# Optimization experiments

Measured on AMD Instinct MI355X. Metric: run time of the kernel, lower is better.

The kernel has to match this reference:

```python
import jax, jax.numpy as jnp
from jax import lax
import numpy as np

ALPHA = 1.0
GAMMA = 1e-6
KBLK = 64  # codebook block size for the L1 NN search scan


def setup_inputs() -> dict:
    key = jax.random.key(0)
    ks = jax.random.split(key, 6)
    B, T, C, F, D, K = 8, 1024, 32, 256, 128, 512
    return {
        "X": jax.random.normal(ks[0], (B, T, C), jnp.float32),
        "H": jax.random.normal(ks[1], (B, D, T), jnp.float32),
        "M": jax.random.normal(ks[2], (D, K), jnp.float32),
        "Hdec": jax.random.normal(ks[3], (B, T, F), jnp.float32),
        "W": jax.random.normal(ks[4], (C, F), jnp.float32) * 0.05,
        "w_d": jax.random.normal(ks[5], (C,), jnp.float32) * 0.05,
    }


def _memory_loss(H, M):
    # H: [B, D, T], M: [D, K]
    Ht = jnp.transpose(H, (0, 2, 1))            # [B, T, D]
    MT = M.T                                     # [K, D] codewords
    K, D = MT.shape
    nblk = K // KBLK
    blocks = MT.reshape(nblk, KBLK, D)
    bases = jnp.arange(nblk, dtype=jnp.int32) * KBLK

    def step(carry, blk_base):
        best_d, best_i = carry
        blk, base = blk_base
        # L1 distance to this block of codewords: [B, T, KBLK]
        d = jnp.sum(jnp.abs(Ht[:, :, None, :] - blk[None, None, :, :]), axis=-1)
        bd = jnp.min(d, axis=-1)
        bi = jnp.argmin(d, axis=-1).astype(jnp.int32) + base
        upd = bd < best_d  # strict < keeps the first (lowest-index) argmin, as torch does
        return (jnp.where(upd, bd, best_d), jnp.where(upd, bi, best_i)), None

    init = (jnp.full(Ht.shape[:2], jnp.inf, Ht.dtype),
            jnp.zeros(Ht.shape[:2], jnp.int32))
    (_, best_i), _ = lax.scan(step, init, (blocks, bases))

    Zt = MT[best_i]  # [B, T, D] gathered nearest codewords
    sg = lax.stop_gradient
    # sum of per-(b,d) squared L2 norms over T == total squared sum
    diffs = jnp.sum((sg(Ht) - Zt) ** 2) + jnp.sum((Ht - sg(Zt)) ** 2)
    return diffs / float(np.prod(H.shape))


def reference(X, H, M, Hdec, W, w_d):
    # decoder last layer + discriminator head (needed for adaptive weight grads)
    def rec_loss(w):
        Xhat = jnp.einsum('btf,cf->btc', Hdec, w)
        return jnp.mean((Xhat - X) ** 2)

    def d_loss(w):
        Xhat = jnp.einsum('btf,cf->btc', Hdec, w)
        return -jnp.mean(Xhat @ w_d)

    loss_rec = rec_loss(W)
    loss_d = d_loss(W)
    loss_m = _memory_loss(H, M)

    g_rec = jax.grad(rec_loss)(W)
    g_d = jax.grad(d_loss)(W)
    lmbda = lax.stop_gradient(
        jnp.linalg.norm(g_rec) / (jnp.linalg.norm(g_d) + GAMMA))

    return loss_rec + ALPHA * loss_m + lmbda * loss_d
```

## Files before the change

kernel.cpp:

```cpp
#include <hip/hip_runtime.h>
#include <hip/hip_bf16.h>
#include <math.h>

#define N_POS 8192
#define D_DIM 128
#define K_DIM 512
#define C_DIM 32
#define F_DIM 256
#define NKT   4
#define GREC_COLS 8448
#define L2_BLOCKS 388
#define XG_BLOCKS 256

__device__ __forceinline__ float block_reduce_256(float v) {
    __shared__ float sbuf[4];
    __syncthreads();
#pragma unroll
    for (int off = 32; off > 0; off >>= 1) v += __shfl_down(v, off);
    const int lane = threadIdx.x & 63;
    const int w    = threadIdx.x >> 6;
    if (lane == 0) sbuf[w] = v;
    __syncthreads();
    return (threadIdx.x == 0) ? (sbuf[0] + sbuf[1] + sbuf[2] + sbuf[3]) : 0.f;
}

__global__ __launch_bounds__(256, 4)
void fused_l1(const float* __restrict__ H, const float* __restrict__ M,
              const float* __restrict__ Hdec, const float* __restrict__ W,
              const float* __restrict__ X, const float* __restrict__ w_d,
              float* __restrict__ MT, float* __restrict__ pd,
              int* __restrict__ pi, float* __restrict__ pp,
              float* __restrict__ accum) {
    __shared__ __align__(16) char smem_raw[38912];
    const int tid = threadIdx.x;

    if (blockIdx.x >= XG_BLOCKS) {
        float* hT = (float*)smem_raw;
        float* mT = hT + 2048;
        float* rd = hT;
        int*   ri = (int*)(hT + 1024);

        const int nb    = blockIdx.x - XG_BLOCKS;
        const int ptile = nb >> 2;
        const int ktile = nb & 3;
        const int pos0  = ptile << 6;
        const int b     = pos0 >> 10;
        const int t0    = pos0 & 1023;
        const int k0    = ktile << 7;
        const float* Hb = H + (b << 17) + t0;

        const int hq = (tid & 15) << 2;
        const int hr = tid >> 4;
        const int mq = (tid & 31) << 2;
        const int mr = tid >> 5;
        const int p4 = (tid & 15) << 2;
        const int q4 = (tid >> 4) << 2;

        float acc[4][8];
#pragma unroll
        for (int i = 0; i < 4; ++i)
#pragma unroll
            for (int j = 0; j < 8; ++j) acc[i][j] = 0.f;

        auto absacc32 = [&](const float4& A,
                            const float4& Ma, const float4& Mc) {
            const float hh[4] = {A.x,  A.y,  A.z,  A.w};
            const float mm[8] = {Ma.x, Ma.y, Ma.z, Ma.w, Mc.x, Mc.y, Mc.z, Mc.w};
#pragma unroll
            for (int i = 0; i < 4; ++i)
#pragma unroll
                for (int j = 0; j < 8; ++j) {
                    const float dv = hh[i] - mm[j];
                    asm("v_add_f32 %0, %0, abs(%1)"
                        : "+v"(acc[i][j]) : "v"(dv));
                }
        };

        const float* hrow = hT + p4;
        const float* mrow = mT + q4;

        for (int ch = 0; ch < 4; ++ch) {
            const int d0 = ch << 5;
            __syncthreads();
#pragma unroll
            for (int p = 0; p < 2; ++p) {
                const int d = (p << 4) + hr;
                *(float4*)(hT + (d << 6) + hq) =
                    *(const float4*)(Hb + ((size_t)(d0 + d) << 10) + hq);
            }
#pragma unroll
            for (int p = 0; p < 4; ++p) {
                const int d = (p << 3) + mr;
                *(float4*)(mT + (d << 7) + mq) =
                    *(const float4*)(M + (size_t)(d0 + d) * K_DIM + k0 + mq);
            }
            __syncthreads();

            float4 ha = *(const float4*)(hrow);
            float4 ma = *(const float4*)(mrow);
            float4 mc = *(const float4*)(mrow + 64);
#pragma unroll 2
            for (int d = 0; d < 31; ++d) {
                const float4 nha = *(const float4*)(hrow + ((d + 1) << 6));
                const float4 nma = *(const float4*)(mrow + ((d + 1) << 7));
                const float4 nmc = *(const float4*)(mrow + ((d + 1) << 7) + 64);
                absacc32(ha, ma, mc);
                ha = nha; ma = nma; mc = nmc;
            }
            absacc32(ha, ma, mc);
        }

        __syncthreads();

#pragma unroll
        for (int i = 0; i < 4; ++i) {
            const int pl = p4 + i;
            float bd = acc[i][0];
            int   bj = 0;
#pragma unroll
            for (int j = 1; j < 8; ++j)
                if (acc[i][j] < bd) { bd = acc[i][j]; bj = j; }
            const int bk = k0 + ((bj < 4) ? (q4 + bj) : (64 + q4 + bj - 4));
            rd[(tid >> 4) * 64 + pl] = bd;
            ri[(tid >> 4) * 64 + pl] = bk;
        }
        __syncthreads();

        if (tid < 64) {
            float bd = rd[tid];
            int   bi = ri[tid];
#pragma unroll
            for (int q = 1; q < 16; ++q) {
                const float d = rd[q * 64 + tid];
                const int   k = ri[q * 64 + tid];
                if (d < bd || (d == bd && k < bi)) { bd = d; bi = k; }
            }
            pd[ktile * N_POS + pos0 + tid] = bd;
            pi[ktile * N_POS + pos0 + tid] = bi;
        }
    } else {
        float* Wl = (float*)smem_raw;
        float* El = Wl + C_DIM * 260;
        const int xb  = blockIdx.x;
        const int bt0 = xb << 5;

        if (xb < 64) {
            const int d0 = xb << 1;
            const int d  = d0 + (tid >> 7);
            const int k  = (tid & 127) << 2;
#pragma unroll
            for (int j = 0; j < 4; ++j)
                MT[(size_t)(k + j) * D_DIM + d] = M[(size_t)d * K_DIM + k + j];
        }

#pragma unroll
        for (int it = 0; it < 8; ++it) {
            const int i = it * 1024 + tid * 4;
            const float4 v = *(const float4*)(W + i);
            *(float4*)(Wl + (i >> 8) * 260 + (i & 255)) = v;
        }
        __syncthreads();

        const int c  = tid & 31;
        const int rg = tid >> 5;
        const int r0 = bt0 + rg, r1 = r0 + 8, r2 = r0 + 16, r3 = r0 + 24;

        float a0 = 0.f, a1 = 0.f, a2 = 0.f, a3 = 0.f;
#pragma unroll 4
        for (int f0 = 0; f0 < F_DIM; f0 += 4) {
            const float4 w4 = *(const float4*)(Wl + c * 260 + f0);
            const float4 h0 = *(const float4*)(Hdec + (size_t)r0 * F_DIM + f0);
            const float4 h1 = *(const float4*)(Hdec + (size_t)r1 * F_DIM + f0);
            const float4 h2 = *(const float4*)(Hdec + (size_t)r2 * F_DIM + f0);
            const float4 h3 = *(const float4*)(Hdec + (size_t)r3 * F_DIM + f0);
            a0 += h0.x * w4.x + h0.y * w4.y + h0.z * w4.z + h0.w * w4.w;
            a1 += h1.x * w4.x + h1.y * w4.y + h1.z * w4.z + h1.w * w4.w;
            a2 += h2.x * w4.x + h2.y * w4.y + h2.z * w4.z + h2.w * w4.w;
            a3 += h3.x * w4.x + h3.y * w4.y + h3.z * w4.z + h3.w * w4.w;
        }

        const float wd = w_d[c];
        const float e0 = a0 - X[(size_t)r0 * C_DIM + c];
        const float e1 = a1 - X[(size_t)r1 * C_DIM + c];
        const float e2 = a2 - X[(size_t)r2 * C_DIM + c];
        const float e3 = a3 - X[(size_t)r3 * C_DIM + c];
        El[(rg)      * 32 + c] = e0;
        El[(rg + 8)  * 32 + c] = e1;
        El[(rg + 16) * 32 + c] = e2;
        El[(rg + 24) * 32 + c] = e3;
        const float sse = e0 * e0 + e1 * e1 + e2 * e2 + e3 * e3;
        const float dp  = (a0 + a1 + a2 + a3) * wd;
        const float rA = block_reduce_256(sse);
        if (tid == 0) atomicAdd(accum + 0, rA);
        const float rB = block_reduce_256(dp);
        if (tid == 0) atomicAdd(accum + 1, rB);
        __syncthreads();

        const int f = tid;
        const float* hp = Hdec + (size_t)bt0 * F_DIM + f;
        float gacc[C_DIM];
#pragma unroll
        for (int cc = 0; cc < C_DIM; ++cc) gacc[cc] = 0.f;
        float sf = 0.f;
        float hd0 = hp[0];
        float hd1 = hp[F_DIM];
#pragma unroll 1
        for (int i = 0; i < 30; ++i) {
            const float hdn = hp[(size_t)(i + 2) * F_DIM];
            sf += hd0;
#pragma unroll
            for (int c4 = 0; c4 < 8; ++c4) {
                const float4 e4 = *(const float4*)(El + i * 32 + c4 * 4);
                gacc[c4 * 4 + 0] += e4.x * hd0;
                gacc[c4 * 4 + 1] += e4.y * hd0;
                gacc[c4 * 4 + 2] += e4.z * hd0;
                gacc[c4 * 4 + 3] += e4.w * hd0;
            }
            hd0 = hd1; hd1 = hdn;
        }
#pragma unroll
        for (int i = 30; i < 32; ++i) {
            sf += hd0;
#pragma unroll
            for (int c4 = 0; c4 < 8; ++c4) {
                const float4 e4 = *(const float4*)(El + i * 32 + c4 * 4);
                gacc[c4 * 4 + 0] += e4.x * hd0;
                gacc[c4 * 4 + 1] += e4.y * hd0;
                gacc[c4 * 4 + 2] += e4.z * hd0;
                gacc[c4 * 4 + 3] += e4.w * hd0;
            }
            hd0 = hd1;
        }
        float* o = pp + (size_t)xb * GREC_COLS;
#pragma unroll
        for (int cc = 0; cc < C_DIM; ++cc) o[cc * F_DIM + f] = gacc[cc];
        o[8192 + f] = sf;
    }
}

__global__ __launch_bounds__(256)
void fused_l2(const float* __restrict__ H, const float* __restrict__ MT,
              const float* __restrict__ pd, const int* __restrict__ pi,
              const float* __restrict__ pp, const float* __restrict__ w_d,
              float* __restrict__ accum, float* __restrict__ out) {
    const int tid = threadIdx.x;
    if (blockIdx.x < 256) {
        const int bx = blockIdx.x & 31;
        const int by = blockIdx.x >> 5;
        const int pos = bx * 256 + tid;
        const int b = pos >> 10;
        const int t = pos & 1023;

        const int d0 = by * 16;
        const float* Hb = H + (b << 17) + t + (d0 << 10);
        float hv[16];
#pragma unroll
        for (int j = 0; j < 16; ++j) hv[j] = Hb[j << 10];

        float bd = INFINITY;
        int   bi = 0x7fffffff;
#pragma unroll
        for (int p = 0; p < NKT; ++p) {
            const float d = pd[p * N_POS + pos];
            const int   k = pi[p * N_POS + pos];
            if (d < bd || (d == bd && k < bi)) { bd = d; bi = k; }
        }

        const float* z  = MT + (size_t)bi * D_DIM + d0;
        const float4 z0 = *(const float4*)(z);
        const float4 z1 = *(const float4*)(z + 4);
        const float4 z2 = *(const float4*)(z + 8);
        const float4 z3 = *(const float4*)(z + 12);
        float s0 = 0.f, s1 = 0.f, s2 = 0.f, s3 = 0.f;
        float e;
        e = hv[0]  - z0.x; s0 += e * e;
        e = hv[1]  - z0.y; s1 += e * e;
        e = hv[2]  - z0.z; s2 += e * e;
        e = hv[3]  - z0.w; s3 += e * e;
        e = hv[4]  - z1.x; s0 += e * e;
        e = hv[5]  - z1.y; s1 += e * e;
        e = hv[6]  - z1.z; s2 += e * e;
        e = hv[7]  - z1.w; s3 += e * e;
        e = hv[8]  - z2.x; s0 += e * e;
        e = hv[9]  - z2.y; s1 += e * e;
        e = hv[10] - z2.z; s2 += e * e;
        e = hv[11] - z2.w; s3 += e * e;
        e = hv[12] - z3.x; s0 += e * e;
        e = hv[13] - z3.y; s1 += e * e;
        e = hv[14] - z3.z; s2 += e * e;
        e = hv[15] - z3.w; s3 += e * e;
        const float r = block_reduce_256((s0 + s1) + (s2 + s3));
        if (tid == 0) atomicAdd(accum + 2, r);
    } else {
        const int g = blockIdx.x - 256;
        const int col = (g < 128) ? (g * 64 + (tid & 63))
                                  : (8192 + (g - 128) * 64 + (tid & 63));
        const int pc  = tid >> 6;
        const float* base = pp + (size_t)(pc * 64) * GREC_COLS + col;
        float s = 0.f;
#pragma unroll 8
        for (int p = 0; p < 64; ++p) s += base[(size_t)p * GREC_COLS];
        __shared__ float red[4][64];
        red[pc][tid & 63] = s;
        __syncthreads();
        if (tid < 64) {
            const float tot = red[0][tid] + red[1][tid] +
                              red[2][tid] + red[3][tid];
            float v = tot * tot;
#pragma unroll
            for (int off = 32; off > 0; off >>= 1) v += __shfl_down(v, off);
            if (tid == 0)
                atomicAdd(accum + ((g >= 128) ? 4 : 3), v);
        }
    }

    __shared__ int is_last;
    if (tid == 0) {
        __threadfence();
        unsigned int* cnt = (unsigned int*)(accum + 5);
        is_last = (atomicAdd(cnt, 1u) == L2_BLOCKS - 1);
    }
    __syncthreads();
    if (is_last && tid < 64) {
        float wd2 = (tid < C_DIM) ? w_d[tid] * w_d[tid] : 0.f;
#pragma unroll
        for (int off = 32; off > 0; off >>= 1) wd2 += __shfl_down(wd2, off);
        if (tid == 0) {
            __threadfence();
            const float sse_rec = atomicAdd(accum + 0, 0.f);
            const float dsum    = atomicAdd(accum + 1, 0.f);
            const float sse_mem = atomicAdd(accum + 2, 0.f);
            const float g2      = atomicAdd(accum + 3, 0.f);
            const float s2      = atomicAdd(accum + 4, 0.f);
            const float loss_rec = sse_rec / 262144.f;
            const float loss_d   = -dsum / 8192.f;
            const float loss_m   = 2.f * sse_mem / 1048576.f;
            const float ngrec    = (2.f / 262144.f) * sqrtf(g2);
            const float ngd      = sqrtf(wd2 * s2) / 8192.f;
            const float lmbda    = ngrec / (ngd + 1e-6f);
            out[0] = loss_rec + loss_m + lmbda * loss_d;
        }
    }
}

extern "C" void kernel_launch(void* const* d_in, const int* in_sizes, int n_in,
                              void* d_out, int out_size, void* d_ws, size_t ws_size,
                              hipStream_t stream) {
    const float* X    = (const float*)d_in[0];
    const float* H    = (const float*)d_in[1];
    const float* M    = (const float*)d_in[2];
    const float* Hdec = (const float*)d_in[3];
    const float* W    = (const float*)d_in[4];
    const float* w_d  = (const float*)d_in[5];

    float* ws    = (float*)d_ws;
    float* MT    = ws;
    float* accum = ws + 65536;
    float* pd    = ws + 65552;
    int*   pi    = (int*)(ws + 98320);
    float* pp    = ws + 131088;

    hipMemsetAsync(accum, 0, 16 * sizeof(float), stream);
    fused_l1<<<768,       256, 0, stream>>>(H, M, Hdec, W, X, w_d,
                                            MT, pd, pi, pp, accum);
    fused_l2<<<L2_BLOCKS, 256, 0, stream>>>(H, MT, pd, pi, pp, w_d,
                                            accum, (float*)d_out);
}
```

Before: 123.4 us.

## Shrink L1 NN tiles to 32 positions and raise occupancy

```diff
diff --git a/kernel.cpp b/kernel.cpp
--- a/kernel.cpp
+++ b/kernel.cpp
@@ -11,6 +11,8 @@
 #define GREC_COLS 8448
 #define L2_BLOCKS 388
 #define XG_BLOCKS 256
+#define NN_BLOCKS 1024
+#define GRID_L1   1280
 
 __device__ __forceinline__ float block_reduce_256(float v) {
     __shared__ float sbuf[4];
@@ -24,123 +26,104 @@
     return (threadIdx.x == 0) ? (sbuf[0] + sbuf[1] + sbuf[2] + sbuf[3]) : 0.f;
 }
 
-__global__ __launch_bounds__(256, 4)
+__global__ __launch_bounds__(256, 6)
 void fused_l1(const float* __restrict__ H, const float* __restrict__ M,
               const float* __restrict__ Hdec, const float* __restrict__ W,
               const float* __restrict__ X, const float* __restrict__ w_d,
               float* __restrict__ MT, float* __restrict__ pd,
               int* __restrict__ pi, float* __restrict__ pp,
               float* __restrict__ accum) {
-    __shared__ __align__(16) char smem_raw[38912];
+    __shared__ __align__(16) float smem[5120];
     const int tid = threadIdx.x;
 
     if (blockIdx.x >= XG_BLOCKS) {
-        float* hT = (float*)smem_raw;
-        float* mT = hT + 2048;
-        float* rd = hT;
-        int*   ri = (int*)(hT + 1024);
+        float* hT = smem;
+        float* mT = smem + 1024;
+        float* rd = smem;
+        int*   ri = (int*)(smem + 1024);
 
         const int nb    = blockIdx.x - XG_BLOCKS;
         const int ptile = nb >> 2;
         const int ktile = nb & 3;
-        const int pos0  = ptile << 6;
+        const int pos0  = ptile << 5;
         const int b     = pos0 >> 10;
         const int t0    = pos0 & 1023;
         const int k0    = ktile << 7;
         const float* Hb = H + (b << 17) + t0;
 
-        const int hq = (tid & 15) << 2;
-        const int hr = tid >> 4;
-        const int mq = (tid & 31) << 2;
-        const int mr = tid >> 5;
-        const int p4 = (tid & 15) << 2;
-        const int q4 = (tid >> 4) << 2;
-
-        float acc[4][8];
+        const int hsr = tid >> 3;
+        const int hsc = (tid & 7) << 2;
+        const int msr = tid >> 5;
+        const int msc = (tid & 31) << 2;
+        const int p4  = (tid & 7) << 2;
+        const int q4  = (tid >> 3) << 2;
+
+        float acc[4][4];
 #pragma unroll
         for (int i = 0; i < 4; ++i)
 #pragma unroll
-            for (int j = 0; j < 8; ++j) acc[i][j] = 0.f;
-
-        auto absacc32 = [&](const float4& A,
-                            const float4& Ma, const float4& Mc) {
-            const float hh[4] = {A.x,  A.y,  A.z,  A.w};
-            const float mm[8] = {Ma.x, Ma.y, Ma.z, Ma.w, Mc.x, Mc.y, Mc.z, Mc.w};
-#pragma unroll
-            for (int i = 0; i < 4; ++i)
-#pragma unroll
-                for (int j = 0; j < 8; ++j) {
-                    const float dv = hh[i] - mm[j];
-                    asm("v_add_f32 %0, %0, abs(%1)"
-                        : "+v"(acc[i][j]) : "v"(dv));
-                }
-        };
-
-        const float* hrow = hT + p4;
-        const float* mrow = mT + q4;
+            for (int j = 0; j < 4; ++j) acc[i][j] = 0.f;
 
         for (int ch = 0; ch < 4; ++ch) {
             const int d0 = ch << 5;
             __syncthreads();
-#pragma unroll
-            for (int p = 0; p < 2; ++p) {
-                const int d = (p << 4) + hr;
-                *(float4*)(hT + (d << 6) + hq) =
-                    *(const float4*)(Hb + ((size_t)(d0 + d) << 10) + hq);
-            }
+            *(float4*)(hT + (hsr << 5) + hsc) =
+                *(const float4*)(Hb + ((size_t)(d0 + hsr) << 10) + hsc);
 #pragma unroll
             for (int p = 0; p < 4; ++p) {
-                const int d = (p << 3) + mr;
-                *(float4*)(mT + (d << 7) + mq) =
-                    *(const float4*)(M + (size_t)(d0 + d) * K_DIM + k0 + mq);
+                const int d = (p << 3) + msr;
+                *(float4*)(mT + (d << 7) + msc) =
+                    *(const float4*)(M + (size_t)(d0 + d) * K_DIM + k0 + msc);
             }
             __syncthreads();
 
-            float4 ha = *(const float4*)(hrow);
-            float4 ma = *(const float4*)(mrow);
-            float4 mc = *(const float4*)(mrow + 64);
-#pragma unroll 2
-            for (int d = 0; d < 31; ++d) {
-                const float4 nha = *(const float4*)(hrow + ((d + 1) << 6));
-                const float4 nma = *(const float4*)(mrow + ((d + 1) << 7));
-                const float4 nmc = *(const float4*)(mrow + ((d + 1) << 7) + 64);
-                absacc32(ha, ma, mc);
-                ha = nha; ma = nma; mc = nmc;
-            }
-            absacc32(ha, ma, mc);
+#pragma unroll 4
+            for (int d = 0; d < 32; ++d) {
+                const float4 ha = *(const float4*)(hT + (d << 5) + p4);
+                const float4 ma = *(const float4*)(mT + (d << 7) + q4);
+                const float hh[4] = {ha.x, ha.y, ha.z, ha.w};
+                const float mm[4] = {ma.x, ma.y, ma.z, ma.w};
+#pragma unroll
+                for (int i = 0; i < 4; ++i)
+#pragma unroll
+                    for (int j = 0; j < 4; ++j) {
+                        const float dv = hh[i] - mm[j];
+                        asm("v_add_f32 %0, %0, abs(%1)"
+                            : "+v"(acc[i][j]) : "v"(dv));
+                    }
+            }
         }
 
         __syncthreads();
 
+        const int kg = tid >> 3;
 #pragma unroll
         for (int i = 0; i < 4; ++i) {
             const int pl = p4 + i;
             float bd = acc[i][0];
             int   bj = 0;
 #pragma unroll
-            for (int j = 1; j < 8; ++j)
+            for (int j = 1; j < 4; ++j)
                 if (acc[i][j] < bd) { bd = acc[i][j]; bj = j; }
-            const int bk = k0 + ((bj < 4) ? (q4 + bj) : (64 + q4 + bj - 4));
-            rd[(tid >> 4) * 64 + pl] = bd;
-            ri[(tid >> 4) * 64 + pl] = bk;
+            rd[kg * 32 + pl] = bd;
+            ri[kg * 32 + pl] = k0 + q4 + bj;
         }
         __syncthreads();
 
-        if (tid < 64) {
+        if (tid < 32) {
             float bd = rd[tid];
             int   bi = ri[tid];
 #pragma unroll
-            for (int q = 1; q < 16; ++q) {
-                const float d = rd[q * 64 + tid];
-                const int   k = ri[q * 64 + tid];
+            for (int q = 1; q < 32; ++q) {
+                const float d = rd[q * 32 + tid];
+                const int   k = ri[q * 32 + tid];
                 if (d < bd || (d == bd && k < bi)) { bd = d; bi = k; }
             }
             pd[ktile * N_POS + pos0 + tid] = bd;
             pi[ktile * N_POS + pos0 + tid] = bi;
         }
     } else {
-        float* Wl = (float*)smem_raw;
-        float* El = Wl + C_DIM * 260;
+        float* El = smem;
         const int xb  = blockIdx.x;
         const int bt0 = xb << 5;
 
@@ -153,22 +136,16 @@
                 MT[(size_t)(k + j) * D_DIM + d] = M[(size_t)d * K_DIM + k + j];
         }
 
-#pragma unroll
-        for (int it = 0; it < 8; ++it) {
-            const int i = it * 1024 + tid * 4;
-            const float4 v = *(const float4*)(W + i);
-            *(float4*)(Wl + (i >> 8) * 260 + (i & 255)) = v;
-        }
-        __syncthreads();
-
         const int c  = tid & 31;
         const int rg = tid >> 5;
         const int r0 = bt0 + rg, r1 = r0 + 8, r2 = r0 + 16, r3 = r0 + 24;
 
+        const float* Wc = W + (size_t)c * F_DIM;
+
         float a0 = 0.f, a1 = 0.f, a2 = 0.f, a3 = 0.f;
 #pragma unroll 4
         for (int f0 = 0; f0 < F_DIM; f0 += 4) {
-            const float4 w4 = *(const float4*)(Wl + c * 260 + f0);
+            const float4 w4 = *(const float4*)(Wc + f0);
             const float4 h0 = *(const float4*)(Hdec + (size_t)r0 * F_DIM + f0);
             const float4 h1 = *(const float4*)(Hdec + (size_t)r1 * F_DIM + f0);
             const float4 h2 = *(const float4*)(Hdec + (size_t)r2 * F_DIM + f0);
@@ -361,7 +338,7 @@
     float* pp    = ws + 131088;
 
     hipMemsetAsync(accum, 0, 16 * sizeof(float), stream);
-    fused_l1<<<768,       256, 0, stream>>>(H, M, Hdec, W, X, w_d,
+    fused_l1<<<GRID_L1,   256, 0, stream>>>(H, M, Hdec, W, X, w_d,
                                             MT, pd, pi, pp, accum);
     fused_l2<<<L2_BLOCKS, 256, 0, stream>>>(H, MT, pd, pi, pp, w_d,
                                             accum, (float*)d_out);
```

New measurement: 124.5 us. No clear change (+0.9%).
